# Kernel optimization log

Hardware: AMD Instinct MI355X
Metric: run time of the kernel (lower is better)

The kernel has to match this reference:

```python
import jax, jax.numpy as jnp
import numpy as np

NEG = -1e20

def _rope(x):
    # x: (N, L, H, D). Original buffers use inv_freq over D with D/2 entries;
    # sin/cos tiled to full D to broadcast (original code's einsum was under-specified for 4D).
    L, D = x.shape[1], x.shape[3]
    inv_freq = 1.0 / (10000.0 ** (jnp.arange(0, D, 2, dtype=jnp.float32) / D))
    t = jnp.arange(L, dtype=jnp.float32)
    freqs = t[:, None] * inv_freq[None, :]            # (L, D/2)
    sin = jnp.concatenate([jnp.sin(freqs)] * 2, -1)[None, :, None, :]  # (1,L,1,D)
    cos = jnp.concatenate([jnp.cos(freqs)] * 2, -1)[None, :, None, :]
    return x * cos + jnp.flip(x, -1) * sin

def setup_inputs() -> dict:
    key = jax.random.key(0)
    ks = jax.random.split(key, 8)
    N, L, E, H = 2, 1024, 2048, 16
    D = E // H
    s = 0.02
    return {
        "values": jax.random.normal(ks[0], (N, L, E), jnp.float32),
        "keys": jax.random.normal(ks[1], (N, L, E), jnp.float32),
        "queries": jax.random.normal(ks[2], (N, L, E), jnp.float32),
        "mask": jax.random.randint(ks[3], (N, 1, L, L), 0, 2, jnp.int32),
        "Wv": jax.random.normal(ks[4], (D, D), jnp.float32) * s,
        "Wk": jax.random.normal(ks[5], (D, D), jnp.float32) * s,
        "Wq": jax.random.normal(ks[6], (D, D), jnp.float32) * s,
        "Wo": jax.random.normal(ks[7], (E, E), jnp.float32) * s,
        "bo": jnp.zeros((E,), jnp.float32),
    }

def reference(values, keys, queries, mask, Wv, Wk, Wq, Wo, bo):
    N, L, E = queries.shape
    H = 16
    D = E // H
    v = values.reshape(N, L, H, D)
    k = keys.reshape(N, L, H, D)
    q = queries.reshape(N, L, H, D)
    q = _rope(q)
    k = _rope(k)
    # per-head linears (nn.Linear: x @ W.T)
    v = jnp.einsum('nlhd,od->nlho', v, Wv)
    k = jnp.einsum('nlhd,od->nlho', k, Wk)
    q = jnp.einsum('nlhd,od->nlho', q, Wq)
    energy = jnp.einsum('nqhd,nkhd->nhqk', q, k)
    energy = jnp.where(mask == 0, NEG, energy)
    attn = jax.nn.softmax(energy / jnp.sqrt(jnp.float32(E)), axis=3)
    out = jnp.einsum('nhqk,nkhd->nqhd', attn, v).reshape(N, L, E)
    return out @ Wo.T + bo
```

## Files before the change

### kernel.cpp

```cpp
#include <hip/hip_runtime.h>

#define LQ 1024
#define EMB 2048
#define NH 16
#define HD 128
#define RSCALE 0.022097086912079608f

typedef unsigned short u16x8 __attribute__((ext_vector_type(8)));
typedef __bf16 bf16x8 __attribute__((ext_vector_type(8)));
typedef float f32x4 __attribute__((ext_vector_type(4)));
typedef short s16x4 __attribute__((ext_vector_type(4)));

typedef const __attribute__((address_space(1))) unsigned int* gas_t;
typedef __attribute__((address_space(3))) unsigned int* las_t;

__device__ __forceinline__ void glds16(const void* g, void* l){
  __builtin_amdgcn_global_load_lds((gas_t)g, (las_t)l, 16, 0, 0);
}
__device__ __forceinline__ unsigned short f2b(float f){
  unsigned int x = __float_as_uint(f);
  return (unsigned short)((x + 0x7fffu + ((x >> 16) & 1u)) >> 16);
}
__device__ __forceinline__ unsigned short f2bu(float f){
  union { __bf16 h; unsigned short u; } c; c.h = (__bf16)f; return c.u;
}
__device__ __forceinline__ short f2bs(float f){
  union { __bf16 h; short s; } c; c.h = (__bf16)f; return c.s;
}
__device__ __forceinline__ bf16x8 as_bf(u16x8 u){
  union { u16x8 u; bf16x8 b; } c; c.u = u; return c.b;
}
__device__ __forceinline__ f32x4 mfma16(s16x4 a, s16x4 b, f32x4 c){
  return __builtin_amdgcn_mfma_f32_16x16x16bf16_1k(a, b, c, 0, 0, 0);
}

__global__ __launch_bounds__(256, 4) void k_proj(
    const float* __restrict__ vals, const float* __restrict__ keys,
    const float* __restrict__ qrys,
    const float* __restrict__ Wv, const float* __restrict__ Wk,
    const float* __restrict__ Wq,
    const float* __restrict__ Wo, const int* __restrict__ M,
    unsigned short* __restrict__ kp, unsigned short* __restrict__ qp,
    unsigned short* __restrict__ vtF, unsigned short* __restrict__ Wob,
    unsigned long long* __restrict__ Mb)
{
  __shared__ unsigned short Xs[64 * 136];
  __shared__ float scC[4 * 128], scS[4 * 128];
  int t = threadIdx.x;
  int which = blockIdx.y;

  if (which == 3) {
    int bx = blockIdx.x;
    #pragma unroll
    for (int k = 0; k < 8; ++k) {
      int i = (bx * 2048 + k * 256 + t) * 4;
      float4 f = *(const float4*)&Wo[i];
      ushort4 u;
      u.x = f2bu(f.x); u.y = f2bu(f.y); u.z = f2bu(f.z); u.w = f2bu(f.w);
      *(ushort4*)&Wob[i] = u;
    }
    int w = t >> 6, lane = t & 63;
    #pragma unroll
    for (int i = 0; i < 16; ++i) {
      int w_idx = bx * 64 + w * 16 + i;
      int n = w_idx >> 14, row = (w_idx >> 4) & 1023, wc = w_idx & 15;
      int v = M[(size_t)n * (LQ * LQ) + (size_t)row * LQ + wc * 64 + lane];
      unsigned long long b = __ballot(v != 0);
      if (lane == 0) Mb[w_idx] = b;
    }
    return;
  }

  const float* X; const float* W; bool rope;
  if (which == 0)      { X = vals; W = Wv; rope = false; }
  else if (which == 1) { X = keys; W = Wk; rope = true;  }
  else                 { X = qrys; W = Wq; rope = true;  }
  float qs = (which == 2) ? RSCALE : 1.0f;

  int w = t >> 6, lane = t & 63, quad = lane >> 4, n16 = lane & 15;

  if (rope) {
    int l0 = (blockIdx.x * 4) & 1023;
    #pragma unroll
    for (int i = 0; i < 2; ++i) {
      int idx = t + 256 * i;
      int li = idx >> 7, d = idx & 127, j = d & 63;
      float inv = 1.0f / powf(10000.0f, (float)(2 * j) * 0.0078125f);
      float ang = (float)(l0 + li) * inv;
      scC[idx] = cosf(ang);
      scS[idx] = sinf(ang);
    }
    __syncthreads();
  }

  if (which == 0) {
    int bh = blockIdx.x >> 4, kt = blockIdx.x & 15;
    int n = bh >> 4, h = bh & 15;
    #pragma unroll
    for (int i = 0; i < 8; ++i) {
      int fi = t + 256 * i;
      int row = fi >> 5, dq = (fi & 31) * 4;
      size_t gr = (size_t)n * 16384 + (size_t)(kt * 64 + row) * 16 + h;
      float4 x = *(const float4*)&X[gr * HD + dq];
      ushort4 u;
      u.x = f2bu(x.x); u.y = f2bu(x.y); u.z = f2bu(x.z); u.w = f2bu(x.w);
      *(ushort4*)&Xs[row * 136 + dq] = u;
    }
  } else {
    int m0 = blockIdx.x * 64;
    #pragma unroll
    for (int i = 0; i < 8; ++i) {
      int fi = t + 256 * i;
      int row = fi >> 5, dq = (fi & 31) * 4;
      int gr = m0 + row;
      float4 x = *(const float4*)&X[(size_t)gr * HD + dq];
      int li = row >> 4;
      float4 xm = *(const float4*)&X[(size_t)gr * HD + (124 - dq)];
      float4 c  = *(const float4*)&scC[li * 128 + dq];
      float4 s  = *(const float4*)&scS[li * 128 + dq];
      ushort4 u;
      u.x = f2bu(x.x * c.x + xm.w * s.x);
      u.y = f2bu(x.y * c.y + xm.z * s.y);
      u.z = f2bu(x.z * c.z + xm.y * s.z);
      u.w = f2bu(x.w * c.w + xm.x * s.w);
      *(ushort4*)&Xs[row * 136 + dq] = u;
    }
  }
  __syncthreads();

  f32x4 of[4][2];
  #pragma unroll
  for (int a = 0; a < 4; ++a)
    { of[a][0] = (f32x4){0.f,0.f,0.f,0.f}; of[a][1] = (f32x4){0.f,0.f,0.f,0.f}; }

  const float* Wr0 = &W[(size_t)(w * 32 + n16) * 128 + quad * 8];
  const float* Wr1 = &W[(size_t)(w * 32 + 16 + n16) * 128 + quad * 8];

  #pragma unroll
  for (int kd = 0; kd < 4; ++kd) {
    float4 a0 = *(const float4*)&Wr0[kd * 32];
    float4 a1 = *(const float4*)&Wr0[kd * 32 + 4];
    float4 b0 = *(const float4*)&Wr1[kd * 32];
    float4 b1 = *(const float4*)&Wr1[kd * 32 + 4];
    u16x8 u0, u1;
    u0[0]=f2bu(a0.x); u0[1]=f2bu(a0.y); u0[2]=f2bu(a0.z); u0[3]=f2bu(a0.w);
    u0[4]=f2bu(a1.x); u0[5]=f2bu(a1.y); u0[6]=f2bu(a1.z); u0[7]=f2bu(a1.w);
    u1[0]=f2bu(b0.x); u1[1]=f2bu(b0.y); u1[2]=f2bu(b0.z); u1[3]=f2bu(b0.w);
    u1[4]=f2bu(b1.x); u1[5]=f2bu(b1.y); u1[6]=f2bu(b1.z); u1[7]=f2bu(b1.w);
    bf16x8 bfr0 = as_bf(u0), bfr1 = as_bf(u1);
    #pragma unroll
    for (int a = 0; a < 4; ++a) {
      bf16x8 af = as_bf(*(const u16x8*)&Xs[(a * 16 + n16) * 136 + kd * 32 + quad * 8]);
      of[a][0] = __builtin_amdgcn_mfma_f32_16x16x32_bf16(af, bfr0, of[a][0], 0, 0, 0);
      of[a][1] = __builtin_amdgcn_mfma_f32_16x16x32_bf16(af, bfr1, of[a][1], 0, 0, 0);
    }
  }

  if (which == 0) {
    int bh = blockIdx.x >> 4, kt = blockIdx.x & 15;
    size_t vbase = (size_t)bh * (LQ * HD) + (size_t)kt * 8192;
    #pragma unroll
    for (int a = 0; a < 4; ++a) {
      #pragma unroll
      for (int b2 = 0; b2 < 2; ++b2) {
        ushort4 u;
        u.x = f2bu(of[a][b2][0]); u.y = f2bu(of[a][b2][1]);
        u.z = f2bu(of[a][b2][2]); u.w = f2bu(of[a][b2][3]);
        *(ushort4*)&vtF[vbase + (size_t)((a * 8 + (w * 2 + b2)) * 256
                                         + (quad * 16 + n16) * 4)] = u;
      }
    }
  } else {
    unsigned short* OUT = (which == 1) ? kp : qp;
    int m0 = blockIdx.x * 64;
    #pragma unroll
    for (int a = 0; a < 4; ++a) {
      #pragma unroll
      for (int b2 = 0; b2 < 2; ++b2) {
        #pragma unroll
        for (int r = 0; r < 4; ++r) {
          int m = m0 + a * 16 + quad * 4 + r;
          int n = m >> 14, l = (m >> 4) & 1023, h = m & 15;
          int o = w * 32 + b2 * 16 + n16;
          OUT[(((size_t)(n * NH + h)) * LQ + l) * HD + o] = f2bu(of[a][b2][r] * qs);
        }
      }
    }
  }
}

__global__ __launch_bounds__(512) void k_attn(
    const unsigned short* __restrict__ qp, const unsigned short* __restrict__ kp,
    const unsigned short* __restrict__ vtF, const unsigned long long* __restrict__ Mb,
    unsigned short* __restrict__ ao)
{
  __shared__ unsigned short KsF[2][8192];
  __shared__ unsigned short VsF[2][8192];
  __shared__ float ls[8][16];
  int t = threadIdx.x, w = t >> 6, lane = t & 63, quad = lane >> 4, n16 = lane & 15;
  int grp = w >> 2, wq = w & 3;
  int lin = blockIdx.y * gridDim.x + blockIdx.x;
  int xcd = lin & 7, j = lin >> 3;
  int bh = xcd + 8 * (j >> 4);
  int q0 = (j & 15) * 64;
  int nIdx = bh >> 4, h = bh & 15;
  size_t base = (size_t)bh * LQ * HD;
  const unsigned short* Q = qp + base;
  const unsigned short* K = kp + base;
  const unsigned short* VF = vtF + base;

  bf16x8 qf[4];
  #pragma unroll
  for (int kd = 0; kd < 4; ++kd)
    qf[kd] = as_bf(*(const u16x8*)&Q[(size_t)(q0 + wq * 16 + n16) * HD + kd * 32 + quad * 8]);

  const unsigned long long* MbRow =
      Mb + ((size_t)nIdx * LQ + q0 + wq * 16 + n16) * 16;

  f32x4 of[8];
  #pragma unroll
  for (int c = 0; c < 8; ++c) of[c] = (f32x4){0.f, 0.f, 0.f, 0.f};
  float lp = 0.f;

  for (int p = 0; p < 8; ++p) {
    int k0 = p * 128;
    __syncthreads();
    #pragma unroll
    for (int jj = 0; jj < 2; ++jj) {
      int kt = 2 * p + jj;
      #pragma unroll
      for (int i = 0; i < 2; ++i) {
        int D = t + 512 * i;
        int nn = D & 15, qq = (D >> 4) & 3, cc = (D >> 6) & 3, kd = D >> 8;
        glds16(&K[(size_t)(k0 + jj * 64 + cc * 16 + nn) * HD + (kd * 4 + qq) * 8],
               &KsF[jj][(size_t)D * 8]);
        glds16(&VF[(size_t)kt * 8192 + (size_t)D * 8],
               &VsF[jj][(size_t)D * 8]);
      }
    }
    unsigned long long mq = MbRow[2 * p + grp];
    __syncthreads();

    unsigned long long msh = mq >> (quad * 4);

    f32x4 sf[4];
    #pragma unroll
    for (int c = 0; c < 4; ++c) sf[c] = (f32x4){0.f, 0.f, 0.f, 0.f};
    __builtin_amdgcn_s_setprio(1);
    #pragma unroll
    for (int kd = 0; kd < 4; ++kd) {
      #pragma unroll
      for (int c = 0; c < 4; ++c) {
        bf16x8 kv = as_bf(*(const u16x8*)&KsF[grp][((kd * 4 + c) * 64 + lane) * 8]);
        sf[c] = __builtin_amdgcn_mfma_f32_16x16x32_bf16(kv, qf[kd], sf[c], 0, 0, 0);
      }
    }
    __builtin_amdgcn_s_setprio(0);
    #pragma unroll
    for (int c = 0; c < 4; ++c) {
      s16x4 pa;
      #pragma unroll
      for (int r = 0; r < 4; ++r) {
        int bit = (int)((msh >> (c * 16 + r)) & 1ull);
        float p = bit ? __expf(sf[c][r]) : 0.f;
        lp += p;
        pa[r] = f2bs(p);
      }
      __builtin_amdgcn_s_setprio(1);
      #pragma unroll
      for (int c2 = 0; c2 < 8; ++c2) {
        s16x4 vv = *(const s16x4*)&VsF[grp][((c * 8 + c2) * 64 + lane) * 4];
        of[c2] = mfma16(pa, vv, of[c2]);
      }
      __builtin_amdgcn_s_setprio(0);
    }
  }

  __syncthreads();
  {
    float s = lp;
    s += __shfl_xor(s, 16);
    s += __shfl_xor(s, 32);
    ls[w][n16] = s;
  }
  float* OF = (float*)&KsF[0][0];
  if (grp == 1) {
    #pragma unroll
    for (int c2 = 0; c2 < 8; ++c2) {
      #pragma unroll
      for (int r = 0; r < 4; ++r) {
        OF[(wq * 16 + quad * 4 + r) * 128 + c2 * 16 + n16] = of[c2][r];
      }
    }
  }
  __syncthreads();
  if (grp == 0) {
    float linv[4];
    #pragma unroll
    for (int r = 0; r < 4; ++r)
      linv[r] = 1.0f / fmaxf(ls[wq][quad * 4 + r] + ls[wq + 4][quad * 4 + r], 1e-30f);
    #pragma unroll
    for (int c2 = 0; c2 < 8; ++c2) {
      #pragma unroll
      for (int r = 0; r < 4; ++r) {
        float v = of[c2][r] + OF[(wq * 16 + quad * 4 + r) * 128 + c2 * 16 + n16];
        ao[((size_t)(nIdx * LQ + q0 + wq * 16 + quad * 4 + r)) * EMB + h * HD + c2 * 16 + n16] =
            f2b(v * linv[r]);
      }
    }
  }
}

__global__ __launch_bounds__(256) void k_outproj(
    const unsigned short* __restrict__ ao, const unsigned short* __restrict__ Wob,
    const float* __restrict__ bo, float* __restrict__ out)
{
  __shared__ unsigned short As[2][128 * 64];
  __shared__ unsigned short Bs[2][64 * 64];
  int t = threadIdx.x;
  int w = t >> 6, lane = t & 63, quad = lane >> 4, n16 = lane & 15;
  int wm = w >> 1, wo = w & 1;
  int m0 = blockIdx.x * 128, o0 = blockIdx.y * 64;
  int ub = (t & 192);

  f32x4 of[4][2];
  #pragma unroll
  for (int a = 0; a < 4; ++a)
    { of[a][0] = (f32x4){0.f,0.f,0.f,0.f}; of[a][1] = (f32x4){0.f,0.f,0.f,0.f}; }

  #pragma unroll
  for (int i = 0; i < 4; ++i) {
    int ci = t + 256 * i;
    int row = ci >> 3, ch = (ci & 7) ^ (row & 7);
    glds16(&ao[(size_t)(m0 + row) * EMB + ch * 8], &As[0][(ub + 256 * i) * 8]);
  }
  #pragma unroll
  for (int i = 0; i < 2; ++i) {
    int ci = t + 256 * i;
    int row = ci >> 3, ch = (ci & 7) ^ (row & 7);
    glds16(&Wob[(size_t)(o0 + row) * EMB + ch * 8], &Bs[0][(ub + 256 * i) * 8]);
  }

  for (int kt = 0; kt < 32; ++kt) {
    int cur = kt & 1;
    __syncthreads();
    if (kt < 31) {
      int k1 = (kt + 1) * 64;
      #pragma unroll
      for (int i = 0; i < 4; ++i) {
        int ci = t + 256 * i;
        int row = ci >> 3, ch = (ci & 7) ^ (row & 7);
        glds16(&ao[(size_t)(m0 + row) * EMB + k1 + ch * 8], &As[1 - cur][(ub + 256 * i) * 8]);
      }
      #pragma unroll
      for (int i = 0; i < 2; ++i) {
        int ci = t + 256 * i;
        int row = ci >> 3, ch = (ci & 7) ^ (row & 7);
        glds16(&Wob[(size_t)(o0 + row) * EMB + k1 + ch * 8], &Bs[1 - cur][(ub + 256 * i) * 8]);
      }
    }
    #pragma unroll
    for (int kd = 0; kd < 2; ++kd) {
      int slot0 = (kd * 4 + quad);
      bf16x8 af[4], bf[2];
      #pragma unroll
      for (int a = 0; a < 4; ++a)
        af[a] = as_bf(*(const u16x8*)&As[cur][(wm * 64 + a * 16 + n16) * 64 + (slot0 ^ (n16 & 7)) * 8]);
      #pragma unroll
      for (int b = 0; b < 2; ++b)
        bf[b] = as_bf(*(const u16x8*)&Bs[cur][(wo * 32 + b * 16 + n16) * 64 + (slot0 ^ (n16 & 7)) * 8]);
      #pragma unroll
      for (int a = 0; a < 4; ++a)
        #pragma unroll
        for (int b = 0; b < 2; ++b)
          of[a][b] = __builtin_amdgcn_mfma_f32_16x16x32_bf16(af[a], bf[b], of[a][b], 0, 0, 0);
    }
  }

  float bb[2] = { bo[o0 + wo * 32 + n16], bo[o0 + wo * 32 + 16 + n16] };
  #pragma unroll
  for (int a = 0; a < 4; ++a) {
    #pragma unroll
    for (int b = 0; b < 2; ++b) {
      #pragma unroll
      for (int r = 0; r < 4; ++r) {
        out[(size_t)(m0 + wm * 64 + a * 16 + quad * 4 + r) * EMB
            + o0 + wo * 32 + b * 16 + n16] = of[a][b][r] + bb[b];
      }
    }
  }
}

extern "C" void kernel_launch(void* const* d_in, const int* in_sizes, int n_in,
                              void* d_out, int out_size, void* d_ws, size_t ws_size,
                              hipStream_t stream) {
  (void)in_sizes; (void)n_in; (void)out_size; (void)ws_size;
  const float* vals = (const float*)d_in[0];
  const float* keys = (const float*)d_in[1];
  const float* qrys = (const float*)d_in[2];
  const int*   mask = (const int*)d_in[3];
  const float* Wv   = (const float*)d_in[4];
  const float* Wk   = (const float*)d_in[5];
  const float* Wq   = (const float*)d_in[6];
  const float* Wo   = (const float*)d_in[7];
  const float* bo   = (const float*)d_in[8];
  float* out = (float*)d_out;

  unsigned short* U  = (unsigned short*)d_ws;
  unsigned short* qp = U;
  unsigned short* kp = U + 4194304;
  unsigned short* vtF= U + 12582912;
  unsigned short* ao = U + 16777216;
  unsigned short* Wob= U + 20971520;
  unsigned long long* Mb = (unsigned long long*)(U + 25165824);

  k_proj    <<<dim3(512, 4), dim3(256), 0, stream>>>(vals, keys, qrys, Wv, Wk, Wq,
                                                     Wo, mask, kp, qp, vtF, Wob, Mb);
  k_attn    <<<dim3(16, 32), dim3(512), 0, stream>>>(qp, kp, vtF, Mb, ao);
  k_outproj <<<dim3(16, 32), dim3(256), 0, stream>>>(ao, Wob, bo, out);
}
```

Before: 199.4 us.

## Enlarge out-projection tile to 128x128 with 512 threads; hoist weight loads in k_proj

The output-projection GEMM moves from a 128x64 tile with 256 threads to a 128x128 tile with 512 threads and 8 waves. This halves the grid and raises arithmetic intensity per block, so each A tile loaded from global is reused across more output columns. Separately, k_proj now issues its per-wave weight loads before the rope and staging phase, overlapping them with that work. It also drops the occupancy hint of 4 in launch bounds, which may raise register pressure and lower occupancy.

```diff
diff --git a/kernel.cpp b/kernel.cpp
--- a/kernel.cpp
+++ b/kernel.cpp
@@ -34,7 +34,7 @@
   return __builtin_amdgcn_mfma_f32_16x16x16bf16_1k(a, b, c, 0, 0, 0);
 }
 
-__global__ __launch_bounds__(256, 4) void k_proj(
+__global__ __launch_bounds__(256) void k_proj(
     const float* __restrict__ vals, const float* __restrict__ keys,
     const float* __restrict__ qrys,
     const float* __restrict__ Wv, const float* __restrict__ Wk,
@@ -78,6 +78,17 @@
   float qs = (which == 2) ? RSCALE : 1.0f;
 
   int w = t >> 6, lane = t & 63, quad = lane >> 4, n16 = lane & 15;
+
+  const float* Wr0 = &W[(size_t)(w * 32 + n16) * 128 + quad * 8];
+  const float* Wr1 = &W[(size_t)(w * 32 + 16 + n16) * 128 + quad * 8];
+  float4 wA0[4], wA1[4], wB0[4], wB1[4];
+  #pragma unroll
+  for (int kd = 0; kd < 4; ++kd) {
+    wA0[kd] = *(const float4*)&Wr0[kd * 32];
+    wA1[kd] = *(const float4*)&Wr0[kd * 32 + 4];
+    wB0[kd] = *(const float4*)&Wr1[kd * 32];
+    wB1[kd] = *(const float4*)&Wr1[kd * 32 + 4];
+  }
 
   if (rope) {
     int l0 = (blockIdx.x * 4) & 1023;
@@ -133,20 +144,13 @@
   for (int a = 0; a < 4; ++a)
     { of[a][0] = (f32x4){0.f,0.f,0.f,0.f}; of[a][1] = (f32x4){0.f,0.f,0.f,0.f}; }
 
-  const float* Wr0 = &W[(size_t)(w * 32 + n16) * 128 + quad * 8];
-  const float* Wr1 = &W[(size_t)(w * 32 + 16 + n16) * 128 + quad * 8];
-
   #pragma unroll
   for (int kd = 0; kd < 4; ++kd) {
-    float4 a0 = *(const float4*)&Wr0[kd * 32];
-    float4 a1 = *(const float4*)&Wr0[kd * 32 + 4];
-    float4 b0 = *(const float4*)&Wr1[kd * 32];
-    float4 b1 = *(const float4*)&Wr1[kd * 32 + 4];
     u16x8 u0, u1;
-    u0[0]=f2bu(a0.x); u0[1]=f2bu(a0.y); u0[2]=f2bu(a0.z); u0[3]=f2bu(a0.w);
-    u0[4]=f2bu(a1.x); u0[5]=f2bu(a1.y); u0[6]=f2bu(a1.z); u0[7]=f2bu(a1.w);
-    u1[0]=f2bu(b0.x); u1[1]=f2bu(b0.y); u1[2]=f2bu(b0.z); u1[3]=f2bu(b0.w);
-    u1[4]=f2bu(b1.x); u1[5]=f2bu(b1.y); u1[6]=f2bu(b1.z); u1[7]=f2bu(b1.w);
+    u0[0]=f2bu(wA0[kd].x); u0[1]=f2bu(wA0[kd].y); u0[2]=f2bu(wA0[kd].z); u0[3]=f2bu(wA0[kd].w);
+    u0[4]=f2bu(wA1[kd].x); u0[5]=f2bu(wA1[kd].y); u0[6]=f2bu(wA1[kd].z); u0[7]=f2bu(wA1[kd].w);
+    u1[0]=f2bu(wB0[kd].x); u1[1]=f2bu(wB0[kd].y); u1[2]=f2bu(wB0[kd].z); u1[3]=f2bu(wB0[kd].w);
+    u1[4]=f2bu(wB1[kd].x); u1[5]=f2bu(wB1[kd].y); u1[6]=f2bu(wB1[kd].z); u1[7]=f2bu(wB1[kd].w);
     bf16x8 bfr0 = as_bf(u0), bfr1 = as_bf(u1);
     #pragma unroll
     for (int a = 0; a < 4; ++a) {
@@ -311,34 +315,30 @@
   }
 }
 
-__global__ __launch_bounds__(256) void k_outproj(
+__global__ __launch_bounds__(512) void k_outproj(
     const unsigned short* __restrict__ ao, const unsigned short* __restrict__ Wob,
     const float* __restrict__ bo, float* __restrict__ out)
 {
   __shared__ unsigned short As[2][128 * 64];
-  __shared__ unsigned short Bs[2][64 * 64];
+  __shared__ unsigned short Bs[2][128 * 64];
   int t = threadIdx.x;
   int w = t >> 6, lane = t & 63, quad = lane >> 4, n16 = lane & 15;
   int wm = w >> 1, wo = w & 1;
-  int m0 = blockIdx.x * 128, o0 = blockIdx.y * 64;
-  int ub = (t & 192);
-
-  f32x4 of[4][2];
-  #pragma unroll
-  for (int a = 0; a < 4; ++a)
-    { of[a][0] = (f32x4){0.f,0.f,0.f,0.f}; of[a][1] = (f32x4){0.f,0.f,0.f,0.f}; }
-
-  #pragma unroll
-  for (int i = 0; i < 4; ++i) {
-    int ci = t + 256 * i;
+  int m0 = blockIdx.x * 128, o0 = blockIdx.y * 128;
+  int ub = (t & 448);
+
+  f32x4 of[2][4];
+  #pragma unroll
+  for (int a = 0; a < 2; ++a)
+    #pragma unroll
+    for (int b = 0; b < 4; ++b) of[a][b] = (f32x4){0.f,0.f,0.f,0.f};
+
+  #pragma unroll
+  for (int i = 0; i < 2; ++i) {
+    int ci = t + 512 * i;
     int row = ci >> 3, ch = (ci & 7) ^ (row & 7);
-    glds16(&ao[(size_t)(m0 + row) * EMB + ch * 8], &As[0][(ub + 256 * i) * 8]);
-  }
-  #pragma unroll
-  for (int i = 0; i < 2; ++i) {
-    int ci = t + 256 * i;
-    int row = ci >> 3, ch = (ci & 7) ^ (row & 7);
-    glds16(&Wob[(size_t)(o0 + row) * EMB + ch * 8], &Bs[0][(ub + 256 * i) * 8]);
+    glds16(&ao[(size_t)(m0 + row) * EMB + ch * 8], &As[0][(ub + 512 * i) * 8]);
+    glds16(&Wob[(size_t)(o0 + row) * EMB + ch * 8], &Bs[0][(ub + 512 * i) * 8]);
   }
 
   for (int kt = 0; kt < 32; ++kt) {
@@ -347,45 +347,42 @@
     if (kt < 31) {
       int k1 = (kt + 1) * 64;
       #pragma unroll
-      for (int i = 0; i < 4; ++i) {
-        int ci = t + 256 * i;
+      for (int i = 0; i < 2; ++i) {
+        int ci = t + 512 * i;
         int row = ci >> 3, ch = (ci & 7) ^ (row & 7);
-        glds16(&ao[(size_t)(m0 + row) * EMB + k1 + ch * 8], &As[1 - cur][(ub + 256 * i) * 8]);
-      }
-      #pragma unroll
-      for (int i = 0; i < 2; ++i) {
-        int ci = t + 256 * i;
-        int row = ci >> 3, ch = (ci & 7) ^ (row & 7);
-        glds16(&Wob[(size_t)(o0 + row) * EMB + k1 + ch * 8], &Bs[1 - cur][(ub + 256 * i) * 8]);
+        glds16(&ao[(size_t)(m0 + row) * EMB + k1 + ch * 8], &As[1 - cur][(ub + 512 * i) * 8]);
+        glds16(&Wob[(size_t)(o0 + row) * EMB + k1 + ch * 8], &Bs[1 - cur][(ub + 512 * i) * 8]);
       }
     }
     #pragma unroll
     for (int kd = 0; kd < 2; ++kd) {
       int slot0 = (kd * 4 + quad);
-      bf16x8 af[4], bf[2];
-      #pragma unroll
-      for (int a = 0; a < 4; ++a)
-        af[a] = as_bf(*(const u16x8*)&As[cur][(wm * 64 + a * 16 + n16) * 64 + (slot0 ^ (n16 & 7)) * 8]);
-      #pragma unroll
-      for (int b = 0; b < 2; ++b)
-        bf[b] = as_bf(*(const u16x8*)&Bs[cur][(wo * 32 + b * 16 + n16) * 64 + (slot0 ^ (n16 & 7)) * 8]);
-      #pragma unroll
-      for (int a = 0; a < 4; ++a)
+      bf16x8 af[2], bf[4];
+      #pragma unroll
+      for (int a = 0; a < 2; ++a)
+        af[a] = as_bf(*(const u16x8*)&As[cur][(wm * 32 + a * 16 + n16) * 64 + (slot0 ^ (n16 & 7)) * 8]);
+      #pragma unroll
+      for (int b = 0; b < 4; ++b)
+        bf[b] = as_bf(*(const u16x8*)&Bs[cur][(wo * 64 + b * 16 + n16) * 64 + (slot0 ^ (n16 & 7)) * 8]);
+      #pragma unroll
+      for (int a = 0; a < 2; ++a)
         #pragma unroll
-        for (int b = 0; b < 2; ++b)
+        for (int b = 0; b < 4; ++b)
           of[a][b] = __builtin_amdgcn_mfma_f32_16x16x32_bf16(af[a], bf[b], of[a][b], 0, 0, 0);
     }
   }
 
-  float bb[2] = { bo[o0 + wo * 32 + n16], bo[o0 + wo * 32 + 16 + n16] };
-  #pragma unroll
-  for (int a = 0; a < 4; ++a) {
-    #pragma unroll
-    for (int b = 0; b < 2; ++b) {
+  float bb[4];
+  #pragma unroll
+  for (int b = 0; b < 4; ++b) bb[b] = bo[o0 + wo * 64 + b * 16 + n16];
+  #pragma unroll
+  for (int a = 0; a < 2; ++a) {
+    #pragma unroll
+    for (int b = 0; b < 4; ++b) {
       #pragma unroll
       for (int r = 0; r < 4; ++r) {
-        out[(size_t)(m0 + wm * 64 + a * 16 + quad * 4 + r) * EMB
-            + o0 + wo * 32 + b * 16 + n16] = of[a][b][r] + bb[b];
+        out[(size_t)(m0 + wm * 32 + a * 16 + quad * 4 + r) * EMB
+            + o0 + wo * 64 + b * 16 + n16] = of[a][b][r] + bb[b];
       }
     }
   }
@@ -417,5 +414,5 @@
   k_proj    <<<dim3(512, 4), dim3(256), 0, stream>>>(vals, keys, qrys, Wv, Wk, Wq,
                                                      Wo, mask, kp, qp, vtF, Wob, Mb);
   k_attn    <<<dim3(16, 32), dim3(512), 0, stream>>>(qp, kp, vtF, Mb, ao);
-  k_outproj <<<dim3(16, 32), dim3(256), 0, stream>>>(ao, Wob, bo, out);
-}
+  k_outproj <<<dim3(16, 16), dim3(512), 0, stream>>>(ao, Wob, bo, out);
+}
```

Result: no change. 202.1 us (+1.4%).
